# Kernel optimization log

Measured on AMD Instinct MI355X. Metric: run time of the kernel, lower is better.

Reference implementation:

```python
import jax, jax.numpy as jnp
import numpy as np

B, S, E, HD = 8, 2048, 1024, 64  # batch, seq, n_embds, head_size (n_embds // n_heads)


def setup_inputs() -> dict:
    key = jax.random.key(0)
    k1, k2, k3, k4 = jax.random.split(key, 4)
    x = jax.random.normal(k1, (B, S, E), dtype=jnp.float32)
    # torch Linear weights have shape [out_features, in_features]; scale like default init
    Wk = jax.random.normal(k2, (HD, E), dtype=jnp.float32) * (1.0 / np.sqrt(E))
    Wq = jax.random.normal(k3, (HD, E), dtype=jnp.float32) * (1.0 / np.sqrt(E))
    Wv = jax.random.normal(k4, (HD, E), dtype=jnp.float32) * (1.0 / np.sqrt(E))
    return {"x": x, "Wk": Wk, "Wq": Wq, "Wv": Wv}


def reference(x, Wk, Wq, Wv):
    # q, k, v: [B, S, HD]
    k = jnp.einsum('bse,he->bsh', x, Wk)
    q = jnp.einsum('bse,he->bsh', x, Wq)
    v = jnp.einsum('bse,he->bsh', x, Wv)
    # scores: [B, S, S], scaled by sqrt(head_size)
    scores = jnp.einsum('bqh,bkh->bqk', q, k) / jnp.sqrt(jnp.float32(HD))
    # causal mask (tril): position q attends to k <= q
    causal = jnp.tril(jnp.ones((S, S), dtype=bool))
    scores = jnp.where(causal, scores, jnp.float32(-jnp.inf))
    attn = jax.nn.softmax(scores, axis=-1)
    # dropout_rate = 0.0 -> identity
    out = jnp.einsum('bqk,bkh->bqh', attn, v)  # [B, S, HD]
    return out
```

## Files before the change

### kernel.cpp

```cpp
#include <hip/hip_runtime.h>
#include <hip/hip_bf16.h>
#include <stdint.h>

typedef short bh8 __attribute__((ext_vector_type(8)));
typedef short bh4 __attribute__((ext_vector_type(4)));
typedef float fx4 __attribute__((ext_vector_type(4)));

#define B_ 8
#define S_ 2048
#define E_ 1024
#define HD_ 64

__device__ __forceinline__ short f2bf(float f) {
  unsigned u = __builtin_bit_cast(unsigned, f);
  u = u + 0x7FFFu + ((u >> 16) & 1u);
  return (short)(u >> 16);
}

#define GL2LDS16(gp, lp) __builtin_amdgcn_global_load_lds( \
    (const __attribute__((address_space(1))) unsigned int*)(gp), \
    (__attribute__((address_space(3))) unsigned int*)(lp), 16, 0, 0)


__global__ __launch_bounds__(256) void castw_k(
    const float* __restrict__ wk, const float* __restrict__ wq,
    const float* __restrict__ wv, short* __restrict__ wc) {
  int i = blockIdx.x * 256 + threadIdx.x;
  int wsel = i >> 13;
  int o = (i & 8191) * 8;
  const float* src = (wsel == 0) ? wk : (wsel == 1) ? wq : wv;
  float4 a = *(const float4*)(src + o);
  float4 b = *(const float4*)(src + o + 4);
  bh8 r = { f2bf(a.x), f2bf(a.y), f2bf(a.z), f2bf(a.w),
            f2bf(b.x), f2bf(b.y), f2bf(b.z), f2bf(b.w) };
  *(bh8*)(wc + wsel * (HD_ * E_) + o) = r;
}

__global__ __launch_bounds__(512) void qkv_gemm(
    const float* __restrict__ x, const short* __restrict__ wc,
    short* __restrict__ kfr, short* __restrict__ qfr, short* __restrict__ vfr) {
  __shared__ short As[2][32 * 32];
  __shared__ short Bs[2][192 * 32];
  const int tid = threadIdx.x;
  const int w = tid >> 6, l = tid & 63;
  const int c = l & 15, g = l >> 4;
  const int r0 = blockIdx.x * 32;
  const int wr = w & 1, wq = w >> 1;
  const int prow = l >> 2;
  const int pcol = (l & 3) * 8;
  const int at = tid - 256;
  const int ar = at >> 3;
  const int ac = (at & 7) * 4;
  const float* xrow = x + (size_t)(r0 + ar) * E_ + ac;

  fx4 acc[3];
  acc[0] = acc[1] = acc[2] = (fx4){0.f, 0.f, 0.f, 0.f};

  float4 xa;
  if (w < 4) {
    GL2LDS16(wc + (size_t)(16 * w + prow) * E_ + pcol, &Bs[0][w * 512]);
    GL2LDS16(wc + (size_t)(16 * (8 + w) + prow) * E_ + pcol, &Bs[0][(8 + w) * 512]);
  } else {
    GL2LDS16(wc + (size_t)(16 * w + prow) * E_ + pcol, &Bs[0][w * 512]);
    xa = *(const float4*)(xrow);
    bh4 aw = { f2bf(xa.x), f2bf(xa.y), f2bf(xa.z), f2bf(xa.w) };
    *(bh4*)&As[0][ar * 32 + ac] = aw;
    __builtin_amdgcn_sched_barrier(0);
    xa = *(const float4*)(xrow + 32);
  }
  __builtin_amdgcn_sched_barrier(0);
  if (w < 4) { asm volatile("s_waitcnt vmcnt(0) lgkmcnt(0)" ::: "memory"); }
  else       { asm volatile("s_waitcnt vmcnt(1) lgkmcnt(0)" ::: "memory"); }
  __builtin_amdgcn_s_barrier();
  __builtin_amdgcn_sched_barrier(0);

  for (int t = 0; t < 32; ++t) {
    const int cur = t & 1;
    if (t < 31) {
      const int k1 = (t + 1) * 32;
      if (w < 4) {
        GL2LDS16(wc + (size_t)(16 * w + prow) * E_ + k1 + pcol, &Bs[cur ^ 1][w * 512]);
        GL2LDS16(wc + (size_t)(16 * (8 + w) + prow) * E_ + k1 + pcol, &Bs[cur ^ 1][(8 + w) * 512]);
      } else {
        GL2LDS16(wc + (size_t)(16 * w + prow) * E_ + k1 + pcol, &Bs[cur ^ 1][w * 512]);
        bh4 aw = { f2bf(xa.x), f2bf(xa.y), f2bf(xa.z), f2bf(xa.w) };
        *(bh4*)&As[cur ^ 1][ar * 32 + ac] = aw;
        __builtin_amdgcn_sched_barrier(0);
        const int k2 = (t + 2 < 32) ? (t + 2) * 32 : 0;
        xa = *(const float4*)(xrow + k2);
      }
      __builtin_amdgcn_sched_barrier(0);
    }

    bh8 af = *(const bh8*)&As[cur][(16 * wr + c) * 32 + 8 * g];
#pragma unroll
    for (int cc = 0; cc < 3; ++cc) {
      bh8 bf = *(const bh8*)&Bs[cur][(16 * (3 * wq + cc) + c) * 32 + 8 * g];
      acc[cc] = __builtin_amdgcn_mfma_f32_16x16x32_bf16(af, bf, acc[cc], 0, 0, 0);
    }

    if (t < 31) {
      __builtin_amdgcn_sched_barrier(0);
      if (w < 4) { asm volatile("s_waitcnt vmcnt(0) lgkmcnt(0)" ::: "memory"); }
      else       { asm volatile("s_waitcnt vmcnt(1) lgkmcnt(0)" ::: "memory"); }
      __builtin_amdgcn_s_barrier();
      __builtin_amdgcn_sched_barrier(0);
    }
  }

  const int rbase = r0 + 16 * wr + 4 * g;
  const int bb = rbase >> 11;
  const int srw = rbase & (S_ - 1);
  const int kt = srw >> 4;
  const int g2 = (srw & 15) >> 2;
#pragma unroll
  for (int cc = 0; cc < 3; ++cc) {
    const int ctg = 3 * wq + cc;
    const int n = 16 * ctg + c;
    if (ctg < 4) {
      const int h = n >> 5, gg = (n & 31) >> 3, jj = n & 7;
      short* dst = kfr + ((size_t)(((bb * 128 + kt) * 2 + h) * 64 + gg * 16) * 8) + jj;
#pragma unroll
      for (int j = 0; j < 4; ++j)
        dst[(size_t)(((rbase + j) & 15)) * 8] = f2bf(acc[cc][j]);
    } else if (ctg < 8) {
      const int nq = n - 64;
      const int h = nq >> 5, gg = (nq & 31) >> 3, jj = nq & 7;
      short* dst = qfr + ((size_t)(((bb * 128 + kt) * 2 + h) * 64 + gg * 16) * 8) + jj;
#pragma unroll
      for (int j = 0; j < 4; ++j)
        dst[(size_t)(((rbase + j) & 15)) * 8] = f2bf(acc[cc][j] * 0.125f);
    } else {
      const int hd = n - 128;
      const int mm = hd >> 4, c2 = hd & 15;
      bh4 pk = { f2bf(acc[cc][0]), f2bf(acc[cc][1]),
                 f2bf(acc[cc][2]), f2bf(acc[cc][3]) };
      *(bh4*)&vfr[(size_t)(((bb * 128 + kt) * 4 + mm) * 64 + g2 * 16 + c2) * 4] = pk;
    }
  }
}

__global__ __launch_bounds__(512, 4) void attn_fused3(
    const short* __restrict__ qfr, const short* __restrict__ kfr,
    const short* __restrict__ vfr, float* __restrict__ out) {
  __shared__ float sO[8][16][68];
  __shared__ float sL[8][16];
  const int tid = threadIdx.x;
  const int w = tid >> 6, l = tid & 63;
  const int c = l & 15, g = l >> 4;
  const int b = blockIdx.x >> 6, p = blockIdx.x & 63;
  const int qtA = p, qtB = 127 - p;

  const short* qbB = qfr + (size_t)(b * 128) * 1024;
  const short* kbB = kfr + (size_t)(b * 128) * 1024;
  const short* vbB = vfr + (size_t)(b * 128) * 1024;

  bh8 qA0 = *(const bh8*)(qbB + (qtA * 2 + 0) * 512 + l * 8);
  bh8 qA1 = *(const bh8*)(qbB + (qtA * 2 + 1) * 512 + l * 8);
  bh8 qB0 = *(const bh8*)(qbB + (qtB * 2 + 0) * 512 + l * 8);
  bh8 qB1 = *(const bh8*)(qbB + (qtB * 2 + 1) * 512 + l * 8);

  fx4 oA[4], oB[4];
#pragma unroll
  for (int mm = 0; mm < 4; ++mm) { oA[mm] = (fx4){0,0,0,0}; oB[mm] = (fx4){0,0,0,0}; }
  float lA = 0.f, lB = 0.f;

  for (int kt = w; kt <= qtB; kt += 8) {
    const short* kp = kbB + kt * 1024;
    bh8 kf0 = *(const bh8*)(kp + l * 8);
    bh8 kf1 = *(const bh8*)(kp + 512 + l * 8);
    const short* vp = vbB + kt * 1024;
    bh4 vf0 = *(const bh4*)(vp + l * 4);
    bh4 vf1 = *(const bh4*)(vp + 256 + l * 4);
    bh4 vf2 = *(const bh4*)(vp + 512 + l * 4);
    bh4 vf3 = *(const bh4*)(vp + 768 + l * 4);

    fx4 sB = {0.f, 0.f, 0.f, 0.f};
    sB = __builtin_amdgcn_mfma_f32_16x16x32_bf16(kf0, qB0, sB, 0, 0, 0);
    sB = __builtin_amdgcn_mfma_f32_16x16x32_bf16(kf1, qB1, sB, 0, 0, 0);
    if (kt == qtB) {
#pragma unroll
      for (int j = 0; j < 4; ++j)
        if (4 * g + j > c) sB[j] = -1e30f;
    }
    const float pB0 = __expf(sB[0] - 8.f);
    const float pB1 = __expf(sB[1] - 8.f);
    const float pB2 = __expf(sB[2] - 8.f);
    const float pB3 = __expf(sB[3] - 8.f);
    lB += (pB0 + pB1) + (pB2 + pB3);
    bh4 pfB = { f2bf(pB0), f2bf(pB1), f2bf(pB2), f2bf(pB3) };
    oB[0] = __builtin_amdgcn_mfma_f32_16x16x16bf16_1k(vf0, pfB, oB[0], 0, 0, 0);
    oB[1] = __builtin_amdgcn_mfma_f32_16x16x16bf16_1k(vf1, pfB, oB[1], 0, 0, 0);
    oB[2] = __builtin_amdgcn_mfma_f32_16x16x16bf16_1k(vf2, pfB, oB[2], 0, 0, 0);
    oB[3] = __builtin_amdgcn_mfma_f32_16x16x16bf16_1k(vf3, pfB, oB[3], 0, 0, 0);

    if (kt <= qtA) {
      fx4 sA = {0.f, 0.f, 0.f, 0.f};
      sA = __builtin_amdgcn_mfma_f32_16x16x32_bf16(kf0, qA0, sA, 0, 0, 0);
      sA = __builtin_amdgcn_mfma_f32_16x16x32_bf16(kf1, qA1, sA, 0, 0, 0);
      if (kt == qtA) {
#pragma unroll
        for (int j = 0; j < 4; ++j)
          if (4 * g + j > c) sA[j] = -1e30f;
      }
      const float pA0 = __expf(sA[0] - 8.f);
      const float pA1 = __expf(sA[1] - 8.f);
      const float pA2 = __expf(sA[2] - 8.f);
      const float pA3 = __expf(sA[3] - 8.f);
      lA += (pA0 + pA1) + (pA2 + pA3);
      bh4 pfA = { f2bf(pA0), f2bf(pA1), f2bf(pA2), f2bf(pA3) };
      oA[0] = __builtin_amdgcn_mfma_f32_16x16x16bf16_1k(vf0, pfA, oA[0], 0, 0, 0);
      oA[1] = __builtin_amdgcn_mfma_f32_16x16x16bf16_1k(vf1, pfA, oA[1], 0, 0, 0);
      oA[2] = __builtin_amdgcn_mfma_f32_16x16x16bf16_1k(vf2, pfA, oA[2], 0, 0, 0);
      oA[3] = __builtin_amdgcn_mfma_f32_16x16x16bf16_1k(vf3, pfA, oA[3], 0, 0, 0);
    }
  }

#pragma unroll
  for (int mm = 0; mm < 4; ++mm)
    *(fx4*)&sO[w][c][16 * mm + 4 * g] = oA[mm];
  lA += __shfl_xor(lA, 16, 64);
  lA += __shfl_xor(lA, 32, 64);
  if (g == 0) sL[w][c] = lA;
  __syncthreads();
  if (w < 4) {
    const int r = tid >> 4;
    const int cg4 = (tid & 15) * 4;
    fx4 a = {0.f, 0.f, 0.f, 0.f};
    float L = 0.f;
#pragma unroll
    for (int i = 0; i < 8; ++i) { a += *(const fx4*)&sO[i][r][cg4]; L += sL[i][r]; }
    fx4 res = a * (1.0f / L);
    *(fx4*)(out + ((size_t)(b * S_ + qtA * 16 + r)) * HD_ + cg4) = res;
  }
  __syncthreads();
#pragma unroll
  for (int mm = 0; mm < 4; ++mm)
    *(fx4*)&sO[w][c][16 * mm + 4 * g] = oB[mm];
  lB += __shfl_xor(lB, 16, 64);
  lB += __shfl_xor(lB, 32, 64);
  if (g == 0) sL[w][c] = lB;
  __syncthreads();
  if (w < 4) {
    const int r = tid >> 4;
    const int cg4 = (tid & 15) * 4;
    fx4 a = {0.f, 0.f, 0.f, 0.f};
    float L = 0.f;
#pragma unroll
    for (int i = 0; i < 8; ++i) { a += *(const fx4*)&sO[i][r][cg4]; L += sL[i][r]; }
    fx4 res = a * (1.0f / L);
    *(fx4*)(out + ((size_t)(b * S_ + qtB * 16 + r)) * HD_ + cg4) = res;
  }
}

extern "C" void kernel_launch(void* const* d_in, const int* in_sizes, int n_in,
                              void* d_out, int out_size, void* d_ws, size_t ws_size,
                              hipStream_t stream) {
  const float* x  = (const float*)d_in[0];
  const float* wk = (const float*)d_in[1];
  const float* wq = (const float*)d_in[2];
  const float* wv = (const float*)d_in[3];
  float* out = (float*)d_out;
  char* ws = (char*)d_ws;
  short* wc  = (short*)(ws);
  short* kfr = (short*)(ws + 393216);
  short* qfr = (short*)(ws + 2490368);
  short* vfr = (short*)(ws + 4587520);

  castw_k<<<dim3(96), dim3(256), 0, stream>>>(wk, wq, wv, wc);
  qkv_gemm<<<dim3(512), dim3(512), 0, stream>>>(x, wc, kfr, qfr, vfr);
  attn_fused3<<<dim3(512), dim3(512), 0, stream>>>(qfr, kfr, vfr, out);
}
```

Before: 48.91 us.

## Double QKV GEMM row tile to 64 rows per block, halving grid

Each QKV projection block now covers 64 rows of x instead of 32. Every wave accumulates six 16x16 output tiles instead of three, the x loads move to 8-wide vectors, and the weight-tile loads are redistributed across waves. This halves how often the shared bf16 weight slab is re-read from L2 and cuts the grid from 512 to 256 blocks. The trade-off is more accumulator registers per wave and fewer blocks, which may underfill the 256 CUs and give less latency hiding.

```diff
diff --git a/kernel.cpp b/kernel.cpp
--- a/kernel.cpp
+++ b/kernel.cpp
@@ -39,38 +39,42 @@
 __global__ __launch_bounds__(512) void qkv_gemm(
     const float* __restrict__ x, const short* __restrict__ wc,
     short* __restrict__ kfr, short* __restrict__ qfr, short* __restrict__ vfr) {
-  __shared__ short As[2][32 * 32];
+  __shared__ short As[2][64 * 32];
   __shared__ short Bs[2][192 * 32];
   const int tid = threadIdx.x;
   const int w = tid >> 6, l = tid & 63;
   const int c = l & 15, g = l >> 4;
-  const int r0 = blockIdx.x * 32;
-  const int wr = w & 1, wq = w >> 1;
+  const int r0 = blockIdx.x * 64;
+  const int wr = w & 3, wq = w >> 2;
   const int prow = l >> 2;
   const int pcol = (l & 3) * 8;
   const int at = tid - 256;
-  const int ar = at >> 3;
-  const int ac = (at & 7) * 4;
-  const float* xrow = x + (size_t)(r0 + ar) * E_ + ac;
-
-  fx4 acc[3];
-  acc[0] = acc[1] = acc[2] = (fx4){0.f, 0.f, 0.f, 0.f};
-
-  float4 xa;
+  const int arow = at >> 2;
+  const int acol = (at & 3) * 8;
+  const float* xrow = x + (size_t)(r0 + arow) * E_ + acol;
+
+  fx4 acc[6];
+#pragma unroll
+  for (int cc = 0; cc < 6; ++cc) acc[cc] = (fx4){0.f, 0.f, 0.f, 0.f};
+
+  float4 xa0, xa1;
   if (w < 4) {
     GL2LDS16(wc + (size_t)(16 * w + prow) * E_ + pcol, &Bs[0][w * 512]);
+    GL2LDS16(wc + (size_t)(16 * (4 + w) + prow) * E_ + pcol, &Bs[0][(4 + w) * 512]);
     GL2LDS16(wc + (size_t)(16 * (8 + w) + prow) * E_ + pcol, &Bs[0][(8 + w) * 512]);
   } else {
-    GL2LDS16(wc + (size_t)(16 * w + prow) * E_ + pcol, &Bs[0][w * 512]);
-    xa = *(const float4*)(xrow);
-    bh4 aw = { f2bf(xa.x), f2bf(xa.y), f2bf(xa.z), f2bf(xa.w) };
-    *(bh4*)&As[0][ar * 32 + ac] = aw;
+    xa0 = *(const float4*)(xrow);
+    xa1 = *(const float4*)(xrow + 4);
+    bh8 aw = { f2bf(xa0.x), f2bf(xa0.y), f2bf(xa0.z), f2bf(xa0.w),
+               f2bf(xa1.x), f2bf(xa1.y), f2bf(xa1.z), f2bf(xa1.w) };
+    *(bh8*)&As[0][arow * 32 + acol] = aw;
     __builtin_amdgcn_sched_barrier(0);
-    xa = *(const float4*)(xrow + 32);
+    xa0 = *(const float4*)(xrow + 32);
+    xa1 = *(const float4*)(xrow + 32 + 4);
   }
   __builtin_amdgcn_sched_barrier(0);
   if (w < 4) { asm volatile("s_waitcnt vmcnt(0) lgkmcnt(0)" ::: "memory"); }
-  else       { asm volatile("s_waitcnt vmcnt(1) lgkmcnt(0)" ::: "memory"); }
+  else       { asm volatile("s_waitcnt vmcnt(2) lgkmcnt(0)" ::: "memory"); }
   __builtin_amdgcn_s_barrier();
   __builtin_amdgcn_sched_barrier(0);
 
@@ -80,29 +84,31 @@
       const int k1 = (t + 1) * 32;
       if (w < 4) {
         GL2LDS16(wc + (size_t)(16 * w + prow) * E_ + k1 + pcol, &Bs[cur ^ 1][w * 512]);
+        GL2LDS16(wc + (size_t)(16 * (4 + w) + prow) * E_ + k1 + pcol, &Bs[cur ^ 1][(4 + w) * 512]);
         GL2LDS16(wc + (size_t)(16 * (8 + w) + prow) * E_ + k1 + pcol, &Bs[cur ^ 1][(8 + w) * 512]);
       } else {
-        GL2LDS16(wc + (size_t)(16 * w + prow) * E_ + k1 + pcol, &Bs[cur ^ 1][w * 512]);
-        bh4 aw = { f2bf(xa.x), f2bf(xa.y), f2bf(xa.z), f2bf(xa.w) };
-        *(bh4*)&As[cur ^ 1][ar * 32 + ac] = aw;
+        bh8 aw = { f2bf(xa0.x), f2bf(xa0.y), f2bf(xa0.z), f2bf(xa0.w),
+                   f2bf(xa1.x), f2bf(xa1.y), f2bf(xa1.z), f2bf(xa1.w) };
+        *(bh8*)&As[cur ^ 1][arow * 32 + acol] = aw;
         __builtin_amdgcn_sched_barrier(0);
         const int k2 = (t + 2 < 32) ? (t + 2) * 32 : 0;
-        xa = *(const float4*)(xrow + k2);
+        xa0 = *(const float4*)(xrow + k2);
+        xa1 = *(const float4*)(xrow + k2 + 4);
       }
       __builtin_amdgcn_sched_barrier(0);
     }
 
     bh8 af = *(const bh8*)&As[cur][(16 * wr + c) * 32 + 8 * g];
 #pragma unroll
-    for (int cc = 0; cc < 3; ++cc) {
-      bh8 bf = *(const bh8*)&Bs[cur][(16 * (3 * wq + cc) + c) * 32 + 8 * g];
+    for (int cc = 0; cc < 6; ++cc) {
+      bh8 bf = *(const bh8*)&Bs[cur][(16 * (6 * wq + cc) + c) * 32 + 8 * g];
       acc[cc] = __builtin_amdgcn_mfma_f32_16x16x32_bf16(af, bf, acc[cc], 0, 0, 0);
     }
 
     if (t < 31) {
       __builtin_amdgcn_sched_barrier(0);
       if (w < 4) { asm volatile("s_waitcnt vmcnt(0) lgkmcnt(0)" ::: "memory"); }
-      else       { asm volatile("s_waitcnt vmcnt(1) lgkmcnt(0)" ::: "memory"); }
+      else       { asm volatile("s_waitcnt vmcnt(2) lgkmcnt(0)" ::: "memory"); }
       __builtin_amdgcn_s_barrier();
       __builtin_amdgcn_sched_barrier(0);
     }
@@ -114,8 +120,8 @@
   const int kt = srw >> 4;
   const int g2 = (srw & 15) >> 2;
 #pragma unroll
-  for (int cc = 0; cc < 3; ++cc) {
-    const int ctg = 3 * wq + cc;
+  for (int cc = 0; cc < 6; ++cc) {
+    const int ctg = 6 * wq + cc;
     const int n = 16 * ctg + c;
     if (ctg < 4) {
       const int h = n >> 5, gg = (n & 31) >> 3, jj = n & 7;
@@ -268,6 +274,6 @@
   short* vfr = (short*)(ws + 4587520);
 
   castw_k<<<dim3(96), dim3(256), 0, stream>>>(wk, wq, wv, wc);
-  qkv_gemm<<<dim3(512), dim3(512), 0, stream>>>(x, wc, kfr, qfr, vfr);
+  qkv_gemm<<<dim3(256), dim3(512), 0, stream>>>(x, wc, kfr, qfr, vfr);
   attn_fused3<<<dim3(512), dim3(512), 0, stream>>>(qfr, kfr, vfr, out);
 }
```

Result: faster. 45.47 us (-7.0%).
